# Optimization experiments

Hardware: AMD Instinct MI355X
Metric: run time of the kernel (lower is better)

Reference implementation:

```python
import jax, jax.numpy as jnp
import numpy as np

N = 1_000_000
C_IN = 32
C_OUT = 32
K = 9  # (1,3,3) kernel -> 9 taps
NEG_SLOPE = 0.01  # nn.LeakyReLU default
BN_EPS = 1e-5


def setup_inputs() -> dict:
    key = jax.random.key(0)
    k1, k2, k3, k4 = jax.random.split(key, 4)
    features = jax.random.normal(k1, (N, C_IN), dtype=jnp.float32)
    weight = jax.random.normal(k2, (K, C_IN, C_OUT), dtype=jnp.float32) * (1.0 / np.sqrt(K * C_IN))
    gamma = jnp.ones((C_OUT,), dtype=jnp.float32)
    beta = jnp.zeros((C_OUT,), dtype=jnp.float32)
    # Rulebook: for each kernel tap, the input voxel index feeding each output voxel.
    neighbor_idx = jax.random.randint(k3, (K, N), 0, N, dtype=jnp.int32)
    neighbor_mask = jax.random.uniform(k4, (K, N)) < 0.7
    # Center tap (k=4 for a 3x3 window) is identity for submanifold conv.
    neighbor_idx = neighbor_idx.at[4].set(jnp.arange(N, dtype=jnp.int32))
    neighbor_mask = neighbor_mask.at[4].set(True)
    return {
        "features": features,
        "weight": weight,
        "gamma": gamma,
        "beta": beta,
        "neighbor_idx": neighbor_idx,
        "neighbor_mask": neighbor_mask,
    }


def reference(features, weight, gamma, beta, neighbor_idx, neighbor_mask):
    # Submanifold sparse conv as rulebook-driven gather -> GEMM -> accumulate.
    out = jnp.zeros((features.shape[0], weight.shape[2]), dtype=features.dtype)
    for k in range(K):  # fixed, small kernel-tap loop (not a data-dim loop)
        gathered = features[neighbor_idx[k]] * neighbor_mask[k][:, None]  # [N, C_in]
        out = out + gathered @ weight[k]  # [N, C_out]
    # LeakyReLU (applied before BN, matching the module)
    y = jnp.where(out >= 0, out, NEG_SLOPE * out)
    # BatchNorm1d (training mode: batch statistics over the N active voxels)
    mean = jnp.mean(y, axis=0)
    var = jnp.mean(jnp.square(y - mean), axis=0)  # biased, as torch BN
    y = (y - mean) * jax.lax.rsqrt(var + BN_EPS) * gamma + beta
    return y
```

## Files before the change

### kernel.cpp

```cpp
#include <hip/hip_runtime.h>
#include <stdint.h>
#include <stddef.h>

#define NN 1000000
#define KT 9
#define NEG_SLOPE 0.01f
#define BN_EPS 1e-5f

typedef float f32x4 __attribute__((ext_vector_type(4)));
typedef short bf16x8 __attribute__((ext_vector_type(8)));

__device__ __forceinline__ short f2bf(float f) {
    union { float f; uint32_t u; } x; x.f = f;
    uint32_t u = x.u;
    uint32_t r = (u + 0x7FFFu + ((u >> 16) & 1u)) >> 16;
    return (short)(r & 0xFFFFu);
}


__global__ void detect_mask_mode_kernel(const uint32_t* __restrict__ mask,
                                        int* __restrict__ flag) {
    if (blockIdx.x == 0 && threadIdx.x == 0) {
        bool anyf = false, anybig = false;
        for (int i = 0; i < 256; ++i) {
            uint32_t w = mask[i];
            if (w == 0x3F800000u) anyf = true;
            else if (w > 1u) anybig = true;
        }
        *flag = anyf ? 2 : (anybig ? 0 : 1);
    }
}

__global__ __launch_bounds__(256) void spconv_kernel(
    const float* __restrict__ feat, const float* __restrict__ wgt,
    const int* __restrict__ nidx, const void* __restrict__ nmask,
    const int* __restrict__ flag, float* __restrict__ out,
    float* __restrict__ stats)
{
    const int mode = *flag;
    const int lane = threadIdx.x & 63;
    const int w    = threadIdx.x >> 6;
    const int col  = lane & 15;
    const int kg   = lane >> 4;
    const int k0   = kg * 8;

    bf16x8 wb[KT][2];
    #pragma unroll
    for (int k = 0; k < KT; ++k) {
        #pragma unroll
        for (int h = 0; h < 2; ++h) {
            bf16x8 b;
            #pragma unroll
            for (int j = 0; j < 8; ++j)
                b[j] = f2bf(wgt[k * 1024 + (k0 + j) * 32 + h * 16 + col]);
            wb[k][h] = b;
        }
    }

    float s0 = 0.f, s1 = 0.f, q0 = 0.f, q1 = 0.f;

    const int gwave = blockIdx.x * 4 + w;
    const int nwave = gridDim.x * 4;
    const int NT = NN / 16;
    const uint8_t* m8  = (const uint8_t*)nmask;
    const int*     m32 = (const int*)nmask;
    const float*   mf  = (const float*)nmask;

    for (int t = gwave; t < NT; t += nwave) {
        const int vbase = t * 16;
        const int v = vbase + col;
        f32x4 acc0 = {0.f, 0.f, 0.f, 0.f};
        f32x4 acc1 = {0.f, 0.f, 0.f, 0.f};
        #pragma unroll
        for (int k = 0; k < KT; ++k) {
            const int e = k * NN + v;
            bool act;
            if (mode == 0)      act = (m8[e]  != 0);
            else if (mode == 1) act = (m32[e] != 0);
            else                act = (mf[e]  != 0.0f);
            bf16x8 a = {0, 0, 0, 0, 0, 0, 0, 0};
            if (act) {
                const int id = nidx[e];
                const float* src = feat + (size_t)id * 32 + k0;
                const f32x4 lo = *(const f32x4*)(src);
                const f32x4 hi = *(const f32x4*)(src + 4);
                #pragma unroll
                for (int j = 0; j < 4; ++j) { a[j] = f2bf(lo[j]); a[j + 4] = f2bf(hi[j]); }
            }
            acc0 = __builtin_amdgcn_mfma_f32_16x16x32_bf16(a, wb[k][0], acc0, 0, 0, 0);
            acc1 = __builtin_amdgcn_mfma_f32_16x16x32_bf16(a, wb[k][1], acc1, 0, 0, 0);
        }
        #pragma unroll
        for (int r = 0; r < 4; ++r) {
            const int row = vbase + kg * 4 + r;
            float y0 = acc0[r]; y0 = (y0 >= 0.f) ? y0 : NEG_SLOPE * y0;
            float y1 = acc1[r]; y1 = (y1 >= 0.f) ? y1 : NEG_SLOPE * y1;
            out[row * 32 + col]      = y0;
            out[row * 32 + 16 + col] = y1;
            s0 += y0; q0 += y0 * y0;
            s1 += y1; q1 += y1 * y1;
        }
    }

    s0 += __shfl_xor(s0, 16); s0 += __shfl_xor(s0, 32);
    s1 += __shfl_xor(s1, 16); s1 += __shfl_xor(s1, 32);
    q0 += __shfl_xor(q0, 16); q0 += __shfl_xor(q0, 32);
    q1 += __shfl_xor(q1, 16); q1 += __shfl_xor(q1, 32);

    __shared__ float red[4][64];
    if (lane < 16) {
        red[w][col]      = s0;  red[w][col + 16] = s1;
        red[w][col + 32] = q0;  red[w][col + 48] = q1;
    }
    __syncthreads();
    if (threadIdx.x < 64) {
        float tot = red[0][threadIdx.x] + red[1][threadIdx.x]
                  + red[2][threadIdx.x] + red[3][threadIdx.x];
        atomicAdd(&stats[threadIdx.x], tot);
    }
}

__global__ void bn_stats_kernel(const float* __restrict__ stats,
                                const float* __restrict__ gamma,
                                const float* __restrict__ beta,
                                float* __restrict__ sc) {
    int c = threadIdx.x;
    if (c < 32) {
        const float inv_n = 1.0f / (float)NN;
        float mean = stats[c] * inv_n;
        float var  = stats[32 + c] * inv_n - mean * mean;
        float s    = gamma[c] * rsqrtf(var + BN_EPS);
        sc[c]      = s;
        sc[32 + c] = beta[c] - mean * s;
    }
}

__global__ __launch_bounds__(256) void bn_apply_kernel(float* __restrict__ out,
                                                       const float* __restrict__ sc) {
    __shared__ float s[32], b[32];
    if (threadIdx.x < 32)      s[threadIdx.x] = sc[threadIdx.x];
    else if (threadIdx.x < 64) b[threadIdx.x - 32] = sc[threadIdx.x];
    __syncthreads();
    f32x4* o4 = (f32x4*)out;
    const int total4 = NN * 32 / 4;
    for (int i = blockIdx.x * blockDim.x + threadIdx.x; i < total4;
         i += gridDim.x * blockDim.x) {
        f32x4 v = o4[i];
        const int c0 = (i & 7) * 4;
        v[0] = v[0] * s[c0]     + b[c0];
        v[1] = v[1] * s[c0 + 1] + b[c0 + 1];
        v[2] = v[2] * s[c0 + 2] + b[c0 + 2];
        v[3] = v[3] * s[c0 + 3] + b[c0 + 3];
        o4[i] = v;
    }
}

extern "C" void kernel_launch(void* const* d_in, const int* in_sizes, int n_in,
                              void* d_out, int out_size, void* d_ws, size_t ws_size,
                              hipStream_t stream) {
    const float* feat  = (const float*)d_in[0];
    const float* wgt   = (const float*)d_in[1];
    const float* gamma = (const float*)d_in[2];
    const float* beta  = (const float*)d_in[3];
    const int*   nidx  = (const int*)d_in[4];
    const void*  nmask = d_in[5];
    float* out = (float*)d_out;
    float* ws  = (float*)d_ws;

    hipMemsetAsync(ws, 0, 64 * sizeof(float), stream);
    detect_mask_mode_kernel<<<1, 64, 0, stream>>>((const uint32_t*)nmask,
                                                  (int*)(ws + 128));
    spconv_kernel<<<1024, 256, 0, stream>>>(feat, wgt, nidx, nmask,
                                            (const int*)(ws + 128), out, ws);
    bn_stats_kernel<<<1, 64, 0, stream>>>(ws, gamma, beta, ws + 64);
    bn_apply_kernel<<<2048, 256, 0, stream>>>(out, ws + 64);
}
```

Measured before the change: 511.9 us.

## Move weights to LDS, prefetch rulebook indices, template mask mode, raise occupancy

The bf16 weight fragments move from 144 per-thread registers into shared memory, which frees registers, and launch bounds now request 6 blocks per CU. All neighbor indices and mask values for a tile are loaded up front, and gathers are issued unconditionally with the result zeroed by the mask. This exposes more memory-level parallelism at the cost of fetching feature rows for inactive neighbors. The mask mode becomes a template parameter, the detect kernel is parallelised with ballot, and the grid sizes of both kernels increase. LDS reads are added in the inner loop, and the extra unmasked gathers raise traffic by about 30%.

```diff
diff --git a/kernel.cpp b/kernel.cpp
--- a/kernel.cpp
+++ b/kernel.cpp
@@ -6,6 +6,7 @@
 #define KT 9
 #define NEG_SLOPE 0.01f
 #define BN_EPS 1e-5f
+#define NTILES (NN / 16)
 
 typedef float f32x4 __attribute__((ext_vector_type(4)));
 typedef short bf16x8 __attribute__((ext_vector_type(8)));
@@ -20,76 +21,62 @@
 
 __global__ void detect_mask_mode_kernel(const uint32_t* __restrict__ mask,
                                         int* __restrict__ flag) {
-    if (blockIdx.x == 0 && threadIdx.x == 0) {
-        bool anyf = false, anybig = false;
-        for (int i = 0; i < 256; ++i) {
-            uint32_t w = mask[i];
-            if (w == 0x3F800000u) anyf = true;
-            else if (w > 1u) anybig = true;
-        }
-        *flag = anyf ? 2 : (anybig ? 0 : 1);
-    }
-}
-
-__global__ __launch_bounds__(256) void spconv_kernel(
-    const float* __restrict__ feat, const float* __restrict__ wgt,
-    const int* __restrict__ nidx, const void* __restrict__ nmask,
-    const int* __restrict__ flag, float* __restrict__ out,
-    float* __restrict__ stats)
+    const int i = threadIdx.x;
+    bool anyf = false, anybig = false;
+    #pragma unroll
+    for (int j = 0; j < 4; ++j) {
+        uint32_t w = mask[i * 4 + j];
+        if (w == 0x3F800000u) anyf = true;
+        else if (w > 1u) anybig = true;
+    }
+    unsigned long long bf = __ballot(anyf);
+    unsigned long long bb = __ballot(anybig);
+    if (i == 0) *flag = bf ? 2 : (bb ? 0 : 1);
+}
+
+template <int MODE>
+__device__ __forceinline__ void conv_loop(
+    const float* __restrict__ feat, const int* __restrict__ nidx,
+    const void* __restrict__ nmask, float* __restrict__ out,
+    const short* wlds, int lane, int col, int kg, int k0,
+    int gwave, int nwave, float& s0, float& s1, float& q0, float& q1)
 {
-    const int mode = *flag;
-    const int lane = threadIdx.x & 63;
-    const int w    = threadIdx.x >> 6;
-    const int col  = lane & 15;
-    const int kg   = lane >> 4;
-    const int k0   = kg * 8;
-
-    bf16x8 wb[KT][2];
-    #pragma unroll
-    for (int k = 0; k < KT; ++k) {
-        #pragma unroll
-        for (int h = 0; h < 2; ++h) {
-            bf16x8 b;
-            #pragma unroll
-            for (int j = 0; j < 8; ++j)
-                b[j] = f2bf(wgt[k * 1024 + (k0 + j) * 32 + h * 16 + col]);
-            wb[k][h] = b;
-        }
-    }
-
-    float s0 = 0.f, s1 = 0.f, q0 = 0.f, q1 = 0.f;
-
-    const int gwave = blockIdx.x * 4 + w;
-    const int nwave = gridDim.x * 4;
-    const int NT = NN / 16;
     const uint8_t* m8  = (const uint8_t*)nmask;
     const int*     m32 = (const int*)nmask;
     const float*   mf  = (const float*)nmask;
 
-    for (int t = gwave; t < NT; t += nwave) {
+    for (int t = gwave; t < NTILES; t += nwave) {
         const int vbase = t * 16;
         const int v = vbase + col;
+
+        int  ids[KT];
+        bool act[KT];
+        #pragma unroll
+        for (int k = 0; k < KT; ++k) {
+            const int e = k * NN + v;
+            ids[k] = nidx[e];
+            if (MODE == 0)      act[k] = (m8[e]  != 0);
+            else if (MODE == 1) act[k] = (m32[e] != 0);
+            else                act[k] = (mf[e]  != 0.0f);
+        }
+
         f32x4 acc0 = {0.f, 0.f, 0.f, 0.f};
         f32x4 acc1 = {0.f, 0.f, 0.f, 0.f};
         #pragma unroll
         for (int k = 0; k < KT; ++k) {
-            const int e = k * NN + v;
-            bool act;
-            if (mode == 0)      act = (m8[e]  != 0);
-            else if (mode == 1) act = (m32[e] != 0);
-            else                act = (mf[e]  != 0.0f);
-            bf16x8 a = {0, 0, 0, 0, 0, 0, 0, 0};
-            if (act) {
-                const int id = nidx[e];
-                const float* src = feat + (size_t)id * 32 + k0;
-                const f32x4 lo = *(const f32x4*)(src);
-                const f32x4 hi = *(const f32x4*)(src + 4);
-                #pragma unroll
-                for (int j = 0; j < 4; ++j) { a[j] = f2bf(lo[j]); a[j + 4] = f2bf(hi[j]); }
-            }
-            acc0 = __builtin_amdgcn_mfma_f32_16x16x32_bf16(a, wb[k][0], acc0, 0, 0, 0);
-            acc1 = __builtin_amdgcn_mfma_f32_16x16x32_bf16(a, wb[k][1], acc1, 0, 0, 0);
+            const float* src = feat + (size_t)ids[k] * 32 + k0;
+            const f32x4 lo = *(const f32x4*)(src);
+            const f32x4 hi = *(const f32x4*)(src + 4);
+            bf16x8 a;
+            #pragma unroll
+            for (int j = 0; j < 4; ++j) { a[j] = f2bf(lo[j]); a[j + 4] = f2bf(hi[j]); }
+            if (!act[k]) a = (bf16x8){0, 0, 0, 0, 0, 0, 0, 0};
+            const bf16x8 b0 = *(const bf16x8*)&wlds[((k * 2 + 0) * 64 + lane) * 8];
+            const bf16x8 b1 = *(const bf16x8*)&wlds[((k * 2 + 1) * 64 + lane) * 8];
+            acc0 = __builtin_amdgcn_mfma_f32_16x16x32_bf16(a, b0, acc0, 0, 0, 0);
+            acc1 = __builtin_amdgcn_mfma_f32_16x16x32_bf16(a, b1, acc1, 0, 0, 0);
         }
+
         #pragma unroll
         for (int r = 0; r < 4; ++r) {
             const int row = vbase + kg * 4 + r;
@@ -101,6 +88,46 @@
             s1 += y1; q1 += y1 * y1;
         }
     }
+}
+
+__global__ __launch_bounds__(256, 6) void spconv_kernel(
+    const float* __restrict__ feat, const float* __restrict__ wgt,
+    const int* __restrict__ nidx, const void* __restrict__ nmask,
+    const int* __restrict__ flag, float* __restrict__ out,
+    float* __restrict__ stats)
+{
+    __shared__ short wlds[KT * 2 * 64 * 8];
+    const int tid = threadIdx.x;
+    for (int s = tid; s < KT * 2 * 64; s += 256) {
+        const int k    = s >> 7;
+        const int rem  = s & 127;
+        const int h    = rem >> 6;
+        const int l2   = rem & 63;
+        const int kg2  = l2 >> 4;
+        const int col2 = l2 & 15;
+        #pragma unroll
+        for (int j = 0; j < 8; ++j)
+            wlds[s * 8 + j] = f2bf(wgt[k * 1024 + (kg2 * 8 + j) * 32 + h * 16 + col2]);
+    }
+    __syncthreads();
+
+    const int mode = *flag;
+    const int lane = threadIdx.x & 63;
+    const int w    = threadIdx.x >> 6;
+    const int col  = lane & 15;
+    const int kg   = lane >> 4;
+    const int k0   = kg * 8;
+
+    const int gwave = blockIdx.x * 4 + w;
+    const int nwave = gridDim.x * 4;
+
+    float s0 = 0.f, s1 = 0.f, q0 = 0.f, q1 = 0.f;
+    if (mode == 0)
+        conv_loop<0>(feat, nidx, nmask, out, wlds, lane, col, kg, k0, gwave, nwave, s0, s1, q0, q1);
+    else if (mode == 1)
+        conv_loop<1>(feat, nidx, nmask, out, wlds, lane, col, kg, k0, gwave, nwave, s0, s1, q0, q1);
+    else
+        conv_loop<2>(feat, nidx, nmask, out, wlds, lane, col, kg, k0, gwave, nwave, s0, s1, q0, q1);
 
     s0 += __shfl_xor(s0, 16); s0 += __shfl_xor(s0, 32);
     s1 += __shfl_xor(s1, 16); s1 += __shfl_xor(s1, 32);
@@ -170,8 +197,8 @@
     hipMemsetAsync(ws, 0, 64 * sizeof(float), stream);
     detect_mask_mode_kernel<<<1, 64, 0, stream>>>((const uint32_t*)nmask,
                                                   (int*)(ws + 128));
-    spconv_kernel<<<1024, 256, 0, stream>>>(feat, wgt, nidx, nmask,
+    spconv_kernel<<<1536, 256, 0, stream>>>(feat, wgt, nidx, nmask,
                                             (const int*)(ws + 128), out, ws);
     bn_stats_kernel<<<1, 64, 0, stream>>>(ws, gamma, beta, ws + 64);
-    bn_apply_kernel<<<2048, 256, 0, stream>>>(out, ws + 64);
-}
+    bn_apply_kernel<<<4096, 256, 0, stream>>>(out, ws + 64);
+}
```

After: 575.4 us. 12.4% more time.
